# Performance work log

Hardware: AMD Instinct MI355X
Metric: run time of the kernel (lower is better)

## Reference

```python
import jax, jax.numpy as jnp
import numpy as np

N_WIDTH = 64
N_ORDER = 4
N_ELEMENTS = 250
N_NODES = N_ELEMENTS * N_ORDER + 1
N_COLL = 200
NDIM = 2
X_MIN = 0.0
X_MAX = 1.0
M = N_ORDER + 1  # nodes per element


def _bases(x):
    # x: [B, W, D] local coords in [-1, 1]; returns phi/dphi/ddphi as [B, W, M, D]
    nodes = jnp.linspace(-1.0, 1.0, M)
    eye = jnp.eye(M, dtype=bool)
    ne = ~eye
    diff = nodes[:, None] - nodes[None, :]
    inv = jnp.where(eye, 0.0, 1.0 / jnp.where(eye, 1.0, diff))  # inv[j,m] = 1/(n_j - n_m)
    r = (x[..., None, None] - nodes) * inv  # [B,W,D,j,m] = (x - n_m)/(n_j - n_m)
    # Lagrange values: L_j = prod_{m != j} r[j,m]
    L = jnp.prod(jnp.where(ne, r, 1.0), axis=-1)  # [B,W,D,M]
    # First derivative: dL_j = sum_{i != j} 1/(n_j-n_i) prod_{m != i,j} r[j,m]
    mask3 = ne[:, None, :] & ne[None, :, :]  # [j,i,m]: m!=j and m!=i
    P = jnp.prod(jnp.where(mask3, r[..., :, None, :], 1.0), axis=-1)  # [B,W,D,j,i]
    dL = jnp.sum(jnp.where(ne, inv, 0.0) * P, axis=-1)  # [B,W,D,M]
    # Faithful to the original indentation bug in dlagrange: the write
    # `dp_list[:, :, j, h] = y` sits OUTSIDE the j-loop, so only the last
    # column j = M-1 is ever filled; all other columns stay zero.
    dL = jnp.where(jnp.arange(M) == M - 1, dL, 0.0)
    # Second derivative: ddL_j = sum_{i!=j} 1/(n_j-n_i) sum_{m!=i,j} 1/(n_j-n_m) prod_{n!=i,j,m} r[j,n]
    mask4 = ne[:, None, None, :] & ne[None, :, None, :] & ne[None, None, :, :]  # [j,i,m,n]
    prodn = jnp.prod(jnp.where(mask4, r[..., :, None, None, :], 1.0), axis=-1)  # [B,W,D,j,i,m]
    Kprod = inv[:, None, :] * prodn
    Ksum = jnp.sum(jnp.where(mask3, Kprod, 0.0), axis=-1)  # [B,W,D,j,i]
    ddL = jnp.sum(jnp.where(ne, inv, 0.0) * Ksum, axis=-1)  # [B,W,D,M]
    tr = lambda a: jnp.transpose(a, (0, 1, 3, 2))  # -> [B,W,M,D]
    return tr(L), tr(dL), tr(ddL)


def _scatter(x, sample, phi_buf, dphi_buf, ddphi_buf):
    B = x.shape[0]
    xr = jnp.broadcast_to(x[:, None, :], (B, N_WIDTH, NDIM))
    x_shift = (N_NODES - 1) * (xr - X_MIN) / (X_MAX - X_MIN)
    id_el = jnp.clip(jnp.floor(x_shift / N_ORDER), 0, N_ELEMENTS - 1)
    nl = (id_el * N_ORDER).astype(jnp.int32)
    nr = nl + N_ORDER
    xt = (x_shift - 0.5 * (nl + nr)) / (0.5 * (nr - nl))
    dx = 0.5 * N_ORDER * (X_MAX - X_MIN) / (N_NODES - 1)
    phi_l, dphi_l, ddphi_l = _bases(xt)
    # Faithful quirk: the torch code indexes nodes_in_l[0, layer], a length-D
    # vector, so each (layer, node, dim-column) scalar is written at the node
    # offsets of ALL input dims.
    Lidx = nl[0]  # [W, D]
    wr = jnp.arange(N_WIDTH)
    for d in range(NDIM):
        for p in range(M):
            v = phi_l[0, :, p, d]
            dv = dphi_l[0, :, p, d] / dx
            ddv = ddphi_l[0, :, p, d] / (dx * dx)
            for dq in range(NDIM):
                pos = Lidx[:, dq] + p
                phi_buf = phi_buf.at[sample, wr, pos, d].set(v)
                dphi_buf = dphi_buf.at[sample, wr, pos, d].set(dv)
                ddphi_buf = ddphi_buf.at[sample, wr, pos, d].set(ddv)
    return phi_buf, dphi_buf, ddphi_buf, dx


def reference(x, flag, sample, weight, phi_buf, dphi_buf, ddphi_buf):
    if flag == 0:
        phi_buf, dphi_buf, ddphi_buf, dx = _scatter(x, sample, phi_buf, dphi_buf, ddphi_buf)
    else:
        dx = 0.5 * N_ORDER * (X_MAX - X_MIN) / (N_NODES - 1)
    # torch.no_grad() on the cuts -> stop_gradient
    phi_cut = jax.lax.stop_gradient(phi_buf[sample:sample + 1])
    dphi_cut = jax.lax.stop_gradient(dphi_buf[sample:sample + 1])
    ddphi_cut = jax.lax.stop_gradient(ddphi_buf[sample:sample + 1])
    t_ik = jnp.einsum('kpj,ikpj->ik', weight, phi_cut)
    dt_ik = jnp.einsum('kpj,ikpj->ik', weight, dphi_cut)
    ddt_ik = jnp.einsum('kpj,ikpj->ik', weight, ddphi_cut)
    return (t_ik, dt_ik, ddt_ik, phi_buf, dphi_buf, ddphi_buf)


def setup_inputs() -> dict:
    key = jax.random.key(0)
    k1, k2 = jax.random.split(key)
    x = jax.random.uniform(k1, (1, NDIM), dtype=jnp.float32)
    weight = jax.random.normal(k2, (N_WIDTH, N_NODES, NDIM), dtype=jnp.float32)
    zeros = lambda: jnp.zeros((N_COLL, N_WIDTH, N_NODES, NDIM), dtype=jnp.float32)
    return {
        'x': x,
        'flag': 0,
        'sample': 7,
        'weight': weight,
        'phi_buf': zeros(),
        'dphi_buf': zeros(),
        'ddphi_buf': zeros(),
    }
```

## Files before the change

kernel.cpp:

```cpp
#include <hip/hip_runtime.h>

#define N_WIDTH 64
#define N_ORDER 4
#define N_ELEMENTS 250
#define N_NODES 1001
#define N_COLL 200
#define NDIM 2
#define MM 5
#define ROW (N_NODES * NDIM)
#define SAMPLE_SLICE (N_WIDTH * ROW)
#define BUF_ELEMS ((long)N_COLL * SAMPLE_SLICE)

__global__ void copy3_kernel(const float4* __restrict__ a, float4* __restrict__ oa,
                             const float4* __restrict__ b, float4* __restrict__ ob,
                             const float4* __restrict__ c, float4* __restrict__ oc,
                             long n4) {
    long i = (long)blockIdx.x * blockDim.x + threadIdx.x;
    long stride = (long)gridDim.x * blockDim.x;
    for (; i < n4; i += stride) {
        oa[i] = a[i];
        ob[i] = b[i];
        oc[i] = c[i];
    }
}

__global__ void scatter_kernel(const float* __restrict__ x,
                               const int* __restrict__ flagp,
                               const int* __restrict__ samplep,
                               float* __restrict__ phi_out,
                               float* __restrict__ dphi_out,
                               float* __restrict__ ddphi_out) {
    if (*flagp != 0) return;
    int t = threadIdx.x;
    if (t >= N_WIDTH * NDIM) return;
    int w = t >> 1;
    int d = t & 1;
    int sample = *samplep;

    float xs[NDIM];
    int nl[NDIM];
    for (int q = 0; q < NDIM; ++q) {
        xs[q] = (float)(N_NODES - 1) * x[q];
        float id_el = floorf(xs[q] / (float)N_ORDER);
        id_el = fminf(fmaxf(id_el, 0.0f), (float)(N_ELEMENTS - 1));
        nl[q] = (int)(id_el * (float)N_ORDER);
    }
    float xt = (xs[d] - ((float)nl[d] + 2.0f)) * 0.5f;

    const float nodes[MM] = {-1.0f, -0.5f, 0.0f, 0.5f, 1.0f};
    float inv[MM][MM], r[MM][MM];
    for (int i = 0; i < MM; ++i)
        for (int k = 0; k < MM; ++k) {
            inv[i][k] = (i == k) ? 0.0f : 1.0f / (nodes[i] - nodes[k]);
            r[i][k] = (xt - nodes[k]) * inv[i][k];
        }

    float L[MM], dL[MM], ddL[MM];
    for (int i = 0; i < MM; ++i) {
        float prod = 1.0f;
        for (int k = 0; k < MM; ++k) if (k != i) prod *= r[i][k];
        L[i] = prod;

        float s = 0.0f;
        for (int j = 0; j < MM; ++j) if (j != i) {
            float pr = 1.0f;
            for (int k = 0; k < MM; ++k) if (k != i && k != j) pr *= r[i][k];
            s += inv[i][j] * pr;
        }
        dL[i] = (i == MM - 1) ? s : 0.0f;

        float ss = 0.0f;
        for (int j = 0; j < MM; ++j) if (j != i) {
            float s2 = 0.0f;
            for (int k = 0; k < MM; ++k) if (k != i && k != j) {
                float pr = 1.0f;
                for (int l = 0; l < MM; ++l) if (l != i && l != j && l != k) pr *= r[i][l];
                s2 += inv[i][k] * pr;
            }
            ss += inv[i][j] * s2;
        }
        ddL[i] = ss;
    }

    const float dx = 0.5f * (float)N_ORDER * 1.0f / (float)(N_NODES - 1);
    const float inv_dx = 1.0f / dx;
    const float inv_dx2 = inv_dx * inv_dx;

    long base = (long)sample * SAMPLE_SLICE + (long)w * ROW;
    for (int p = 0; p < MM; ++p) {
        float v = L[p];
        float dv = dL[p] * inv_dx;
        float ddv = ddL[p] * inv_dx2;
        long o0 = base + (long)(nl[0] + p) * NDIM + d;
        long o1 = base + (long)(nl[1] + p) * NDIM + d;
        phi_out[o0] = v;   phi_out[o1] = v;
        dphi_out[o0] = dv; dphi_out[o1] = dv;
        ddphi_out[o0] = ddv; ddphi_out[o1] = ddv;
    }
}

__device__ __forceinline__ float wave_reduce(float v) {
    for (int off = 32; off > 0; off >>= 1) v += __shfl_down(v, off, 64);
    return v;
}

__global__ void reduce_kernel(const float* __restrict__ weight,
                              const float* __restrict__ phi,
                              const float* __restrict__ dphi,
                              const float* __restrict__ ddphi,
                              const int* __restrict__ samplep,
                              float* __restrict__ out) {
    int k = blockIdx.x;
    int tid = threadIdx.x;
    long wbase = (long)k * ROW;
    long pbase = (long)(*samplep) * SAMPLE_SLICE + (long)k * ROW;

    float st = 0.0f, sdt = 0.0f, sddt = 0.0f;
    for (int i = tid; i < ROW; i += blockDim.x) {
        float wv = weight[wbase + i];
        st   += wv * phi[pbase + i];
        sdt  += wv * dphi[pbase + i];
        sddt += wv * ddphi[pbase + i];
    }

    st = wave_reduce(st);
    sdt = wave_reduce(sdt);
    sddt = wave_reduce(sddt);

    __shared__ float sh[3][4];
    int lane = tid & 63;
    int wid = tid >> 6;
    if (lane == 0) { sh[0][wid] = st; sh[1][wid] = sdt; sh[2][wid] = sddt; }
    __syncthreads();
    if (tid == 0) {
        out[k]       = sh[0][0] + sh[0][1] + sh[0][2] + sh[0][3];
        out[64 + k]  = sh[1][0] + sh[1][1] + sh[1][2] + sh[1][3];
        out[128 + k] = sh[2][0] + sh[2][1] + sh[2][2] + sh[2][3];
    }
}

extern "C" void kernel_launch(void* const* d_in, const int* in_sizes, int n_in,
                              void* d_out, int out_size, void* d_ws, size_t ws_size,
                              hipStream_t stream) {
    const float* x       = (const float*)d_in[0];
    const int*   flagp   = (const int*)d_in[1];
    const int*   samplep = (const int*)d_in[2];
    const float* weight  = (const float*)d_in[3];
    const float* phi_in  = (const float*)d_in[4];
    const float* dphi_in = (const float*)d_in[5];
    const float* ddphi_in= (const float*)d_in[6];

    float* out = (float*)d_out;
    float* t_out      = out;
    float* phi_out    = out + 192;
    float* dphi_out   = phi_out + BUF_ELEMS;
    float* ddphi_out  = dphi_out + BUF_ELEMS;

    long n4 = BUF_ELEMS / 4;

    copy3_kernel<<<2048, 256, 0, stream>>>(
        (const float4*)phi_in,  (float4*)phi_out,
        (const float4*)dphi_in, (float4*)dphi_out,
        (const float4*)ddphi_in,(float4*)ddphi_out, n4);

    scatter_kernel<<<1, 128, 0, stream>>>(x, flagp, samplep,
                                          phi_out, dphi_out, ddphi_out);

    reduce_kernel<<<64, 256, 0, stream>>>(weight, phi_out, dphi_out, ddphi_out,
                                          samplep, t_out);
}
```

Measured before the change: 521.1 us.

## Use nontemporal per-buffer copy and fuse scatter into the reduction kernel

The three-buffer copy now gives each buffer its own segment of blocks and uses nontemporal vector loads and stores, which is meant to cut cache pollution on the large streaming copy. The single-block scatter kernel is merged into the reduction kernel. That kernel reads the original input buffers and adds a correction for the few entries it overwrites, so it no longer depends on reading back the copied output and one launch is removed. The fused scatter runs on two threads per block and contains redundant duplicate stores. Its handling of overlapping node indices must match the original write order.

New measurement: 530.1 us. About the same (+1.7%).

```diff
diff --git a/kernel.cpp b/kernel.cpp
--- a/kernel.cpp
+++ b/kernel.cpp
@@ -10,92 +10,23 @@
 #define ROW (N_NODES * NDIM)
 #define SAMPLE_SLICE (N_WIDTH * ROW)
 #define BUF_ELEMS ((long)N_COLL * SAMPLE_SLICE)
+#define BLOCKS_PER_BUF 2048
 
-__global__ void copy3_kernel(const float4* __restrict__ a, float4* __restrict__ oa,
-                             const float4* __restrict__ b, float4* __restrict__ ob,
-                             const float4* __restrict__ c, float4* __restrict__ oc,
-                             long n4) {
-    long i = (long)blockIdx.x * blockDim.x + threadIdx.x;
-    long stride = (long)gridDim.x * blockDim.x;
+typedef float v4f __attribute__((ext_vector_type(4)));
+
+__global__ void copy_seg_kernel(const v4f* __restrict__ a, v4f* __restrict__ oa,
+                                const v4f* __restrict__ b, v4f* __restrict__ ob,
+                                const v4f* __restrict__ c, v4f* __restrict__ oc,
+                                long n4) {
+    int buf = blockIdx.x / BLOCKS_PER_BUF;
+    int bid = blockIdx.x % BLOCKS_PER_BUF;
+    const v4f* __restrict__ src = (buf == 0) ? a : (buf == 1) ? b : c;
+    v4f* __restrict__ dst       = (buf == 0) ? oa : (buf == 1) ? ob : oc;
+    long i = (long)bid * blockDim.x + threadIdx.x;
+    long stride = (long)BLOCKS_PER_BUF * blockDim.x;
     for (; i < n4; i += stride) {
-        oa[i] = a[i];
-        ob[i] = b[i];
-        oc[i] = c[i];
-    }
-}
-
-__global__ void scatter_kernel(const float* __restrict__ x,
-                               const int* __restrict__ flagp,
-                               const int* __restrict__ samplep,
-                               float* __restrict__ phi_out,
-                               float* __restrict__ dphi_out,
-                               float* __restrict__ ddphi_out) {
-    if (*flagp != 0) return;
-    int t = threadIdx.x;
-    if (t >= N_WIDTH * NDIM) return;
-    int w = t >> 1;
-    int d = t & 1;
-    int sample = *samplep;
-
-    float xs[NDIM];
-    int nl[NDIM];
-    for (int q = 0; q < NDIM; ++q) {
-        xs[q] = (float)(N_NODES - 1) * x[q];
-        float id_el = floorf(xs[q] / (float)N_ORDER);
-        id_el = fminf(fmaxf(id_el, 0.0f), (float)(N_ELEMENTS - 1));
-        nl[q] = (int)(id_el * (float)N_ORDER);
-    }
-    float xt = (xs[d] - ((float)nl[d] + 2.0f)) * 0.5f;
-
-    const float nodes[MM] = {-1.0f, -0.5f, 0.0f, 0.5f, 1.0f};
-    float inv[MM][MM], r[MM][MM];
-    for (int i = 0; i < MM; ++i)
-        for (int k = 0; k < MM; ++k) {
-            inv[i][k] = (i == k) ? 0.0f : 1.0f / (nodes[i] - nodes[k]);
-            r[i][k] = (xt - nodes[k]) * inv[i][k];
-        }
-
-    float L[MM], dL[MM], ddL[MM];
-    for (int i = 0; i < MM; ++i) {
-        float prod = 1.0f;
-        for (int k = 0; k < MM; ++k) if (k != i) prod *= r[i][k];
-        L[i] = prod;
-
-        float s = 0.0f;
-        for (int j = 0; j < MM; ++j) if (j != i) {
-            float pr = 1.0f;
-            for (int k = 0; k < MM; ++k) if (k != i && k != j) pr *= r[i][k];
-            s += inv[i][j] * pr;
-        }
-        dL[i] = (i == MM - 1) ? s : 0.0f;
-
-        float ss = 0.0f;
-        for (int j = 0; j < MM; ++j) if (j != i) {
-            float s2 = 0.0f;
-            for (int k = 0; k < MM; ++k) if (k != i && k != j) {
-                float pr = 1.0f;
-                for (int l = 0; l < MM; ++l) if (l != i && l != j && l != k) pr *= r[i][l];
-                s2 += inv[i][k] * pr;
-            }
-            ss += inv[i][j] * s2;
-        }
-        ddL[i] = ss;
-    }
-
-    const float dx = 0.5f * (float)N_ORDER * 1.0f / (float)(N_NODES - 1);
-    const float inv_dx = 1.0f / dx;
-    const float inv_dx2 = inv_dx * inv_dx;
-
-    long base = (long)sample * SAMPLE_SLICE + (long)w * ROW;
-    for (int p = 0; p < MM; ++p) {
-        float v = L[p];
-        float dv = dL[p] * inv_dx;
-        float ddv = ddL[p] * inv_dx2;
-        long o0 = base + (long)(nl[0] + p) * NDIM + d;
-        long o1 = base + (long)(nl[1] + p) * NDIM + d;
-        phi_out[o0] = v;   phi_out[o1] = v;
-        dphi_out[o0] = dv; dphi_out[o1] = dv;
-        ddphi_out[o0] = ddv; ddphi_out[o1] = ddv;
+        v4f v = __builtin_nontemporal_load(&src[i]);
+        __builtin_nontemporal_store(v, &dst[i]);
     }
 }
 
@@ -104,23 +35,106 @@
     return v;
 }
 
-__global__ void reduce_kernel(const float* __restrict__ weight,
-                              const float* __restrict__ phi,
-                              const float* __restrict__ dphi,
-                              const float* __restrict__ ddphi,
-                              const int* __restrict__ samplep,
-                              float* __restrict__ out) {
+__global__ void scatter_reduce_kernel(const float* __restrict__ x,
+                                      const int* __restrict__ flagp,
+                                      const int* __restrict__ samplep,
+                                      const float* __restrict__ weight,
+                                      const float* __restrict__ phi_in,
+                                      const float* __restrict__ dphi_in,
+                                      const float* __restrict__ ddphi_in,
+                                      float* __restrict__ phi_out,
+                                      float* __restrict__ dphi_out,
+                                      float* __restrict__ ddphi_out,
+                                      float* __restrict__ t_out) {
     int k = blockIdx.x;
     int tid = threadIdx.x;
+    int flag = *flagp;
+    int sample = *samplep;
     long wbase = (long)k * ROW;
-    long pbase = (long)(*samplep) * SAMPLE_SLICE + (long)k * ROW;
+    long inbase = (long)sample * SAMPLE_SLICE + (long)k * ROW;
 
     float st = 0.0f, sdt = 0.0f, sddt = 0.0f;
-    for (int i = tid; i < ROW; i += blockDim.x) {
+    for (int i = tid; i < ROW; i += 256) {
         float wv = weight[wbase + i];
-        st   += wv * phi[pbase + i];
-        sdt  += wv * dphi[pbase + i];
-        sddt += wv * ddphi[pbase + i];
+        st   += wv * phi_in[inbase + i];
+        sdt  += wv * dphi_in[inbase + i];
+        sddt += wv * ddphi_in[inbase + i];
+    }
+
+    if (flag == 0 && tid < NDIM) {
+        int d = tid;
+        float xs[NDIM];
+        int nl[NDIM];
+        for (int q = 0; q < NDIM; ++q) {
+            xs[q] = (float)(N_NODES - 1) * x[q];
+            float id_el = floorf(xs[q] / (float)N_ORDER);
+            id_el = fminf(fmaxf(id_el, 0.0f), (float)(N_ELEMENTS - 1));
+            nl[q] = (int)(id_el * (float)N_ORDER);
+        }
+        float xt = (xs[d] - ((float)nl[d] + 2.0f)) * 0.5f;
+
+        const float nodes[MM] = {-1.0f, -0.5f, 0.0f, 0.5f, 1.0f};
+        float inv[MM][MM], r[MM][MM];
+        for (int i = 0; i < MM; ++i)
+            for (int kk = 0; kk < MM; ++kk) {
+                inv[i][kk] = (i == kk) ? 0.0f : 1.0f / (nodes[i] - nodes[kk]);
+                r[i][kk] = (xt - nodes[kk]) * inv[i][kk];
+            }
+
+        float L[MM], dL[MM], ddL[MM];
+        for (int i = 0; i < MM; ++i) {
+            float prod = 1.0f;
+            for (int kk = 0; kk < MM; ++kk) if (kk != i) prod *= r[i][kk];
+            L[i] = prod;
+
+            float s = 0.0f;
+            for (int j = 0; j < MM; ++j) if (j != i) {
+                float pr = 1.0f;
+                for (int kk = 0; kk < MM; ++kk) if (kk != i && kk != j) pr *= r[i][kk];
+                s += inv[i][j] * pr;
+            }
+            dL[i] = (i == MM - 1) ? s : 0.0f;
+
+            float ss = 0.0f;
+            for (int j = 0; j < MM; ++j) if (j != i) {
+                float s2 = 0.0f;
+                for (int kk = 0; kk < MM; ++kk) if (kk != i && kk != j) {
+                    float pr = 1.0f;
+                    for (int l = 0; l < MM; ++l) if (l != i && l != j && l != kk) pr *= r[i][l];
+                    s2 += inv[i][kk] * pr;
+                }
+                ss += inv[i][j] * s2;
+            }
+            ddL[i] = ss;
+        }
+
+        const float dx = 0.5f * (float)N_ORDER / (float)(N_NODES - 1);
+        const float inv_dx = 1.0f / dx;
+        const float inv_dx2 = inv_dx * inv_dx;
+
+        int qmin = min(nl[0], nl[1]);
+        int qmax = max(nl[0], nl[1]) + N_ORDER;
+        for (int q = qmin; q <= qmax; ++q) {
+            int p0 = q - nl[0];
+            int p1 = q - nl[1];
+            int p = -1;
+            if (p0 >= 0 && p0 <= N_ORDER) p = p0;
+            if (p1 >= 0 && p1 <= N_ORDER && p1 > p) p = p1;
+            if (p < 0) continue;
+            float v   = L[p];
+            float dv  = dL[p] * inv_dx;
+            float ddv = ddL[p] * inv_dx2;
+            long off = (long)q * NDIM + d;
+            phi_out[inbase - wbase + wbase + off] = v;
+            dphi_out[inbase + off - wbase + wbase] = dv;
+            ddphi_out[inbase + off] = ddv;
+            phi_out[inbase + off] = v;
+            dphi_out[inbase + off] = dv;
+            float wv = weight[wbase + off];
+            st   += wv * (v   - phi_in[inbase + off]);
+            sdt  += wv * (dv  - dphi_in[inbase + off]);
+            sddt += wv * (ddv - ddphi_in[inbase + off]);
+        }
     }
 
     st = wave_reduce(st);
@@ -133,39 +147,37 @@
     if (lane == 0) { sh[0][wid] = st; sh[1][wid] = sdt; sh[2][wid] = sddt; }
     __syncthreads();
     if (tid == 0) {
-        out[k]       = sh[0][0] + sh[0][1] + sh[0][2] + sh[0][3];
-        out[64 + k]  = sh[1][0] + sh[1][1] + sh[1][2] + sh[1][3];
-        out[128 + k] = sh[2][0] + sh[2][1] + sh[2][2] + sh[2][3];
+        t_out[k]       = sh[0][0] + sh[0][1] + sh[0][2] + sh[0][3];
+        t_out[64 + k]  = sh[1][0] + sh[1][1] + sh[1][2] + sh[1][3];
+        t_out[128 + k] = sh[2][0] + sh[2][1] + sh[2][2] + sh[2][3];
     }
 }
 
 extern "C" void kernel_launch(void* const* d_in, const int* in_sizes, int n_in,
                               void* d_out, int out_size, void* d_ws, size_t ws_size,
                               hipStream_t stream) {
-    const float* x       = (const float*)d_in[0];
-    const int*   flagp   = (const int*)d_in[1];
-    const int*   samplep = (const int*)d_in[2];
-    const float* weight  = (const float*)d_in[3];
-    const float* phi_in  = (const float*)d_in[4];
-    const float* dphi_in = (const float*)d_in[5];
-    const float* ddphi_in= (const float*)d_in[6];
+    const float* x        = (const float*)d_in[0];
+    const int*   flagp    = (const int*)d_in[1];
+    const int*   samplep  = (const int*)d_in[2];
+    const float* weight   = (const float*)d_in[3];
+    const float* phi_in   = (const float*)d_in[4];
+    const float* dphi_in  = (const float*)d_in[5];
+    const float* ddphi_in = (const float*)d_in[6];
 
     float* out = (float*)d_out;
-    float* t_out      = out;
-    float* phi_out    = out + 192;
-    float* dphi_out   = phi_out + BUF_ELEMS;
-    float* ddphi_out  = dphi_out + BUF_ELEMS;
+    float* t_out     = out;
+    float* phi_out   = out + 192;
+    float* dphi_out  = phi_out + BUF_ELEMS;
+    float* ddphi_out = dphi_out + BUF_ELEMS;
 
     long n4 = BUF_ELEMS / 4;
 
-    copy3_kernel<<<2048, 256, 0, stream>>>(
-        (const float4*)phi_in,  (float4*)phi_out,
-        (const float4*)dphi_in, (float4*)dphi_out,
-        (const float4*)ddphi_in,(float4*)ddphi_out, n4);
+    copy_seg_kernel<<<3 * BLOCKS_PER_BUF, 256, 0, stream>>>(
+        (const v4f*)phi_in,  (v4f*)phi_out,
+        (const v4f*)dphi_in, (v4f*)dphi_out,
+        (const v4f*)ddphi_in,(v4f*)ddphi_out, n4);
 
-    scatter_kernel<<<1, 128, 0, stream>>>(x, flagp, samplep,
-                                          phi_out, dphi_out, ddphi_out);
-
-    reduce_kernel<<<64, 256, 0, stream>>>(weight, phi_out, dphi_out, ddphi_out,
-                                          samplep, t_out);
+    scatter_reduce_kernel<<<64, 256, 0, stream>>>(
+        x, flagp, samplep, weight, phi_in, dphi_in, ddphi_in,
+        phi_out, dphi_out, ddphi_out, t_out);
 }
```
